# Performance work log

Hardware: AMD Instinct MI355X
Metric: run time of the kernel (lower is better)

The kernel has to match this reference:

```python
import jax, jax.numpy as jnp
import numpy as np

# Constant from livnium.kernel.constants (assumed scalar; value taken as 1.0).
K_O = 1.0
EPS = 1e-12  # F.normalize default eps

B, D, C = 16384, 1024, 3
F_DIM = D + 10  # features = h_final (D) + 10 scalar features


def setup_inputs() -> dict:
    key = jax.random.key(0)
    ks = jax.random.split(key, 8)
    s1 = 1.0 / np.sqrt(F_DIM)
    return {
        "h_final": jax.random.normal(ks[0], (B, D), jnp.float32),
        "v_p": jax.random.normal(ks[1], (B, D), jnp.float32),
        "v_h": jax.random.normal(ks[2], (B, D), jnp.float32),
        "neutral_dir": jax.random.normal(ks[3], (D,), jnp.float32),
        "neutral_scale": jnp.array(1.0, jnp.float32),
        "w1": jax.random.normal(ks[4], (F_DIM, F_DIM), jnp.float32) * s1,
        "b1": jnp.zeros((F_DIM,), jnp.float32),
        "w2": jax.random.normal(ks[5], (C, F_DIM), jnp.float32) * s1,
        "b2": jnp.zeros((C,), jnp.float32),
    }


def _normalize(x, axis):
    n = jnp.linalg.norm(x, axis=axis, keepdims=True)
    return x / jnp.maximum(n, EPS)


def reference(h_final, v_p, v_h, neutral_dir, neutral_scale, w1, b1, w2, b2):
    v_p_n = _normalize(v_p, -1)                      # [B, D]
    v_h_n = _normalize(v_h, -1)                      # [B, D]
    nd_n = _normalize(neutral_dir, 0)                # [D]

    # alignment(): cosine of the unit vectors == batched dot product.
    align = jnp.sum(v_p_n * v_h_n, axis=-1, keepdims=True)        # [B, 1]
    opp = jnp.sum(-v_p_n * v_h_n, axis=-1, keepdims=True)          # [B, 1]
    align_neutral_p = neutral_scale * jnp.sum(v_p_n * nd_n, axis=-1, keepdims=True)
    align_neutral_h = neutral_scale * jnp.sum(v_h_n * nd_n, axis=-1, keepdims=True)

    energy = K_O * ((1.0 + align) * 0.5)
    expose_neg = (1.0 - align) * 0.5
    dist_p_h = jnp.linalg.norm(v_h - v_p, axis=-1, keepdims=True)
    r_p = jnp.linalg.norm(v_p, axis=-1, keepdims=True)
    r_h = jnp.linalg.norm(v_h, axis=-1, keepdims=True)
    r_final = jnp.linalg.norm(h_final, axis=-1, keepdims=True)

    features = jnp.concatenate(
        [h_final, align, opp, energy, expose_neg, dist_p_h,
         r_p, r_h, r_final, align_neutral_p, align_neutral_h], axis=-1)  # [B, D+10]

    hidden = jax.nn.relu(features @ w1.T + b1)
    logits = hidden @ w2.T + b2                      # [B, C]
    return logits
```

## Files before the change

### kernel.cpp

```cpp
#include <hip/hip_runtime.h>
#include <cstdint>
#include <cstddef>

#define B_ROWS 16384
#define D_DIM  1024
#define F_REAL 1034
#define N_PAD  1152
#define K_PAD  1088
#define NK     (K_PAD / 64)
#define EPSN   1e-12f

typedef __bf16 bf16x8 __attribute__((ext_vector_type(8)));
typedef float  f32x4  __attribute__((ext_vector_type(4)));
typedef unsigned short u16;

__device__ __forceinline__ u16 f2bf(float f) {
    __bf16 b = (__bf16)f;
    return __builtin_bit_cast(u16, b);
}

__global__ __launch_bounds__(256)
void prep_kernel(const float* __restrict__ h, const float* __restrict__ vp,
                 const float* __restrict__ vh, const float* __restrict__ nd,
                 const float* __restrict__ nsp, u16* __restrict__ A)
{
    const int row  = blockIdx.x * 4 + (threadIdx.x >> 6);
    const int lane = threadIdx.x & 63;
    const float4* hp  = (const float4*)(h  + (size_t)row * D_DIM);
    const float4* vpp = (const float4*)(vp + (size_t)row * D_DIM);
    const float4* vhp = (const float4*)(vh + (size_t)row * D_DIM);
    const float4* ndp = (const float4*)nd;
    u16* arow = A + (size_t)row * K_PAD;

    float s_pp = 0.f, s_hh = 0.f, s_pv = 0.f, s_ff = 0.f;
    float s_dd = 0.f, s_pn = 0.f, s_hn = 0.f, s_nn = 0.f;

    #pragma unroll
    for (int c = 0; c < 4; ++c) {
        const int idx = lane + c * 64;
        float4 p = vpp[idx], q = vhp[idx], f = hp[idx], n = ndp[idx];

        s_pp += p.x*p.x + p.y*p.y + p.z*p.z + p.w*p.w;
        s_hh += q.x*q.x + q.y*q.y + q.z*q.z + q.w*q.w;
        s_pv += p.x*q.x + p.y*q.y + p.z*q.z + p.w*q.w;
        s_ff += f.x*f.x + f.y*f.y + f.z*f.z + f.w*f.w;
        float dx = q.x-p.x, dy = q.y-p.y, dz = q.z-p.z, dw = q.w-p.w;
        s_dd += dx*dx + dy*dy + dz*dz + dw*dw;
        s_pn += p.x*n.x + p.y*n.y + p.z*n.z + p.w*n.w;
        s_hn += q.x*n.x + q.y*n.y + q.z*n.z + q.w*n.w;
        s_nn += n.x*n.x + n.y*n.y + n.z*n.z + n.w*n.w;

        ushort4 ho;
        ho.x = f2bf(f.x); ho.y = f2bf(f.y); ho.z = f2bf(f.z); ho.w = f2bf(f.w);
        *(ushort4*)(arow + idx * 4) = ho;
    }

    #pragma unroll
    for (int m = 32; m >= 1; m >>= 1) {
        s_pp += __shfl_xor(s_pp, m, 64);
        s_hh += __shfl_xor(s_hh, m, 64);
        s_pv += __shfl_xor(s_pv, m, 64);
        s_ff += __shfl_xor(s_ff, m, 64);
        s_dd += __shfl_xor(s_dd, m, 64);
        s_pn += __shfl_xor(s_pn, m, 64);
        s_hn += __shfl_xor(s_hn, m, 64);
        s_nn += __shfl_xor(s_nn, m, 64);
    }

    if (lane == 0) {
        float np_ = sqrtf(s_pp), nh_ = sqrtf(s_hh), nf = sqrtf(s_ff);
        float npc = fmaxf(np_, EPSN), nhc = fmaxf(nh_, EPSN);
        float nnc = fmaxf(sqrtf(s_nn), EPSN);
        float align = s_pv / (npc * nhc);
        float ns = nsp[0];
        u16 fo[64];
        fo[0] = f2bf(align);
        fo[1] = f2bf(-align);
        fo[2] = f2bf(0.5f * (1.0f + align));
        fo[3] = f2bf(0.5f * (1.0f - align));
        fo[4] = f2bf(sqrtf(s_dd));
        fo[5] = f2bf(np_);
        fo[6] = f2bf(nh_);
        fo[7] = f2bf(nf);
        fo[8] = f2bf(ns * s_pn / (npc * nnc));
        fo[9] = f2bf(ns * s_hn / (nhc * nnc));
        #pragma unroll
        for (int i = 10; i < 64; ++i) fo[i] = 0;
        #pragma unroll
        for (int i = 0; i < 8; ++i)
            *(uint4*)(arow + D_DIM + i * 8) = *(uint4*)(fo + i * 8);
    }
}

__global__ __launch_bounds__(256)
void convw_kernel(const float* __restrict__ w1, u16* __restrict__ Bm)
{
    const int i = blockIdx.x;
    for (int j = threadIdx.x; j < K_PAD; j += 256) {
        float v = (i < F_REAL && j < F_REAL) ? w1[(size_t)i * F_REAL + j] : 0.0f;
        Bm[(size_t)i * K_PAD + j] = f2bf(v);
    }
}

__global__ __launch_bounds__(256)
void initout_kernel(const float* __restrict__ b2, float* __restrict__ out)
{
    int i = blockIdx.x * 256 + threadIdx.x;
    if (i < B_ROWS * 3) out[i] = b2[i % 3];
}

__global__ __launch_bounds__(256)
void gemm_kernel(const u16* __restrict__ A,
                 const u16* __restrict__ Bm,
                 const float* __restrict__ b1, const float* __restrict__ w2,
                 float* __restrict__ out)
{
    __shared__ __bf16 As[2 * 64 * 32];
    __shared__ __bf16 Bs[2 * 128 * 32];

    const int tid  = threadIdx.x;
    const int lane = tid & 63;
    const int wave = tid >> 6;
    const int wm = wave >> 1, wn = wave & 1;
    const int bm = blockIdx.x, bn = blockIdx.y;

    const u16* gaA;
    __bf16*    lA;
    {
        int row = tid >> 2;
        int kc  = (tid & 3) ^ (row & 3);
        gaA = A + (size_t)(bm * 64 + row) * K_PAD + kc * 8;
        lA  = As + tid * 8;
    }
    const u16* gaB[2];
    __bf16*    lB[2];
    #pragma unroll
    for (int o = 0; o < 2; ++o) {
        int s   = o * 256 + tid;
        int row = s >> 2;
        int kc  = (s & 3) ^ (row & 3);
        gaB[o] = Bm + (size_t)(bn * 128 + row) * K_PAD + kc * 8;
        lB[o]  = Bs + s * 8;
    }

    const int col  = lane & 15;
    const int quad = lane >> 4;
    const int swz  = quad ^ (col & 3);
    int aoff[2], boff[4];
    #pragma unroll
    for (int i = 0; i < 2; ++i)
        aoff[i] = ((wm * 32 + i * 16 + col) * 4 + swz) * 8;
    #pragma unroll
    for (int j = 0; j < 4; ++j)
        boff[j] = ((wn * 64 + j * 16 + col) * 4 + swz) * 8;

    f32x4 acc[2][4];
    #pragma unroll
    for (int i = 0; i < 2; ++i)
        #pragma unroll
        for (int j = 0; j < 4; ++j)
            acc[i][j] = (f32x4){0.f, 0.f, 0.f, 0.f};

    uint4 ra0, ra1, rb00, rb01, rb10, rb11;
    ra0  = *(const uint4*)(gaA);
    ra1  = *(const uint4*)(gaA + 32);
    rb00 = *(const uint4*)(gaB[0]);
    rb01 = *(const uint4*)(gaB[0] + 32);
    rb10 = *(const uint4*)(gaB[1]);
    rb11 = *(const uint4*)(gaB[1] + 32);
    *(uint4*)(lA)            = ra0;
    *(uint4*)(lA + 2048)     = ra1;
    *(uint4*)(lB[0])         = rb00;
    *(uint4*)(lB[0] + 4096)  = rb01;
    *(uint4*)(lB[1])         = rb10;
    *(uint4*)(lB[1] + 4096)  = rb11;
    __syncthreads();

    for (int kt = 0; kt < NK; ++kt) {
        if (kt + 1 < NK) {
            const int ko = (kt + 1) * 64;
            ra0  = *(const uint4*)(gaA + ko);
            ra1  = *(const uint4*)(gaA + ko + 32);
            rb00 = *(const uint4*)(gaB[0] + ko);
            rb01 = *(const uint4*)(gaB[0] + ko + 32);
            rb10 = *(const uint4*)(gaB[1] + ko);
            rb11 = *(const uint4*)(gaB[1] + ko + 32);
        }

        #pragma unroll
        for (int h = 0; h < 2; ++h) {
            const __bf16* Ab = As + h * 2048;
            const __bf16* Bb = Bs + h * 4096;
            bf16x8 av[2], bv[4];
            #pragma unroll
            for (int i = 0; i < 2; ++i) av[i] = *(const bf16x8*)(Ab + aoff[i]);
            #pragma unroll
            for (int j = 0; j < 4; ++j) bv[j] = *(const bf16x8*)(Bb + boff[j]);
            #pragma unroll
            for (int i = 0; i < 2; ++i)
                #pragma unroll
                for (int j = 0; j < 4; ++j)
                    acc[i][j] = __builtin_amdgcn_mfma_f32_16x16x32_bf16(
                                    av[i], bv[j], acc[i][j], 0, 0, 0);
        }

        if (kt + 1 < NK) {
            __syncthreads();
            *(uint4*)(lA)            = ra0;
            *(uint4*)(lA + 2048)     = ra1;
            *(uint4*)(lB[0])         = rb00;
            *(uint4*)(lB[0] + 4096)  = rb01;
            *(uint4*)(lB[1])         = rb10;
            *(uint4*)(lB[1] + 4096)  = rb11;
            __syncthreads();
        }
    }

    float bias[4], w20[4], w21[4], w22[4];
    #pragma unroll
    for (int ni = 0; ni < 4; ++ni) {
        int n = bn * 128 + wn * 64 + ni * 16 + col;
        bool v = n < F_REAL;
        bias[ni] = v ? b1[n] : 0.0f;
        w20[ni]  = v ? w2[n] : 0.0f;
        w21[ni]  = v ? w2[F_REAL + n] : 0.0f;
        w22[ni]  = v ? w2[2 * F_REAL + n] : 0.0f;
    }
    #pragma unroll
    for (int mi = 0; mi < 2; ++mi) {
        float c0[4] = {0,0,0,0}, c1[4] = {0,0,0,0}, c2[4] = {0,0,0,0};
        #pragma unroll
        for (int ni = 0; ni < 4; ++ni) {
            #pragma unroll
            for (int r = 0; r < 4; ++r) {
                float hd = fmaxf(acc[mi][ni][r] + bias[ni], 0.0f);
                c0[r] += hd * w20[ni];
                c1[r] += hd * w21[ni];
                c2[r] += hd * w22[ni];
            }
        }
        #pragma unroll
        for (int m = 8; m >= 1; m >>= 1) {
            #pragma unroll
            for (int r = 0; r < 4; ++r) {
                c0[r] += __shfl_xor(c0[r], m, 64);
                c1[r] += __shfl_xor(c1[r], m, 64);
                c2[r] += __shfl_xor(c2[r], m, 64);
            }
        }
        if (col == 0) {
            int gm = bm * 64 + wm * 32 + mi * 16 + quad * 4;
            #pragma unroll
            for (int r = 0; r < 4; ++r) {
                atomicAdd(out + (size_t)(gm + r) * 3 + 0, c0[r]);
                atomicAdd(out + (size_t)(gm + r) * 3 + 1, c1[r]);
                atomicAdd(out + (size_t)(gm + r) * 3 + 2, c2[r]);
            }
        }
    }
}

extern "C" void kernel_launch(void* const* d_in, const int* in_sizes, int n_in,
                              void* d_out, int out_size, void* d_ws, size_t ws_size,
                              hipStream_t stream)
{
    const float* h  = (const float*)d_in[0];
    const float* vp = (const float*)d_in[1];
    const float* vh = (const float*)d_in[2];
    const float* nd = (const float*)d_in[3];
    const float* ns = (const float*)d_in[4];
    const float* w1 = (const float*)d_in[5];
    const float* b1 = (const float*)d_in[6];
    const float* w2 = (const float*)d_in[7];
    const float* b2 = (const float*)d_in[8];
    float* out = (float*)d_out;

    u16* Afull = (u16*)d_ws;
    u16* Bfull = Afull + (size_t)B_ROWS * K_PAD;

    prep_kernel<<<B_ROWS / 4, 256, 0, stream>>>(h, vp, vh, nd, ns, Afull);
    convw_kernel<<<N_PAD, 256, 0, stream>>>(w1, Bfull);
    initout_kernel<<<(B_ROWS * 3 + 255) / 256, 256, 0, stream>>>(b2, out);
    gemm_kernel<<<dim3(B_ROWS / 64, N_PAD / 128), 256, 0, stream>>>(
        Afull, Bfull, b1, w2, out);
}
```

Baseline: 299.5 us.

## Double-buffer GEMM LDS tiles, swap grid order, and batch prep loads

The GEMM kernel now uses two LDS buffers so the next k-tile is written into the alternate buffer, which removes one barrier per iteration. The grid axes are swapped so consecutive blocks share the same A row-tile, aiming for better L2 reuse of A. In the prep kernel, all global loads are issued before any compute to increase memory-level parallelism. The cost is doubled LDS use, which may reduce occupancy.

```diff
diff --git a/kernel.cpp b/kernel.cpp
--- a/kernel.cpp
+++ b/kernel.cpp
@@ -32,14 +32,22 @@
     const float4* ndp = (const float4*)nd;
     u16* arow = A + (size_t)row * K_PAD;
 
+    float4 pr[4], qr[4], fr[4], nr[4];
+    #pragma unroll
+    for (int c = 0; c < 4; ++c) pr[c] = vpp[lane + c * 64];
+    #pragma unroll
+    for (int c = 0; c < 4; ++c) qr[c] = vhp[lane + c * 64];
+    #pragma unroll
+    for (int c = 0; c < 4; ++c) fr[c] = hp[lane + c * 64];
+    #pragma unroll
+    for (int c = 0; c < 4; ++c) nr[c] = ndp[lane + c * 64];
+
     float s_pp = 0.f, s_hh = 0.f, s_pv = 0.f, s_ff = 0.f;
     float s_dd = 0.f, s_pn = 0.f, s_hn = 0.f, s_nn = 0.f;
 
     #pragma unroll
     for (int c = 0; c < 4; ++c) {
-        const int idx = lane + c * 64;
-        float4 p = vpp[idx], q = vhp[idx], f = hp[idx], n = ndp[idx];
-
+        float4 p = pr[c], q = qr[c], f = fr[c], n = nr[c];
         s_pp += p.x*p.x + p.y*p.y + p.z*p.z + p.w*p.w;
         s_hh += q.x*q.x + q.y*q.y + q.z*q.z + q.w*q.w;
         s_pv += p.x*q.x + p.y*q.y + p.z*q.z + p.w*q.w;
@@ -52,7 +60,7 @@
 
         ushort4 ho;
         ho.x = f2bf(f.x); ho.y = f2bf(f.y); ho.z = f2bf(f.z); ho.w = f2bf(f.w);
-        *(ushort4*)(arow + idx * 4) = ho;
+        *(ushort4*)(arow + (lane + c * 64) * 4) = ho;
     }
 
     #pragma unroll
@@ -115,32 +123,32 @@
                  const float* __restrict__ b1, const float* __restrict__ w2,
                  float* __restrict__ out)
 {
-    __shared__ __bf16 As[2 * 64 * 32];
-    __shared__ __bf16 Bs[2 * 128 * 32];
+    __shared__ __bf16 As[2][2 * 64 * 32];
+    __shared__ __bf16 Bs[2][2 * 128 * 32];
 
     const int tid  = threadIdx.x;
     const int lane = tid & 63;
     const int wave = tid >> 6;
     const int wm = wave >> 1, wn = wave & 1;
-    const int bm = blockIdx.x, bn = blockIdx.y;
+    const int bn = blockIdx.x, bm = blockIdx.y;
 
     const u16* gaA;
-    __bf16*    lA;
+    int slotA;
     {
         int row = tid >> 2;
         int kc  = (tid & 3) ^ (row & 3);
-        gaA = A + (size_t)(bm * 64 + row) * K_PAD + kc * 8;
-        lA  = As + tid * 8;
+        gaA   = A + (size_t)(bm * 64 + row) * K_PAD + kc * 8;
+        slotA = tid * 8;
     }
     const u16* gaB[2];
-    __bf16*    lB[2];
+    int slotB[2];
     #pragma unroll
     for (int o = 0; o < 2; ++o) {
         int s   = o * 256 + tid;
         int row = s >> 2;
         int kc  = (s & 3) ^ (row & 3);
-        gaB[o] = Bm + (size_t)(bn * 128 + row) * K_PAD + kc * 8;
-        lB[o]  = Bs + s * 8;
+        gaB[o]   = Bm + (size_t)(bn * 128 + row) * K_PAD + kc * 8;
+        slotB[o] = s * 8;
     }
 
     const int col  = lane & 15;
@@ -168,15 +176,17 @@
     rb01 = *(const uint4*)(gaB[0] + 32);
     rb10 = *(const uint4*)(gaB[1]);
     rb11 = *(const uint4*)(gaB[1] + 32);
-    *(uint4*)(lA)            = ra0;
-    *(uint4*)(lA + 2048)     = ra1;
-    *(uint4*)(lB[0])         = rb00;
-    *(uint4*)(lB[0] + 4096)  = rb01;
-    *(uint4*)(lB[1])         = rb10;
-    *(uint4*)(lB[1] + 4096)  = rb11;
+    *(uint4*)(&As[0][slotA])           = ra0;
+    *(uint4*)(&As[0][slotA + 2048])    = ra1;
+    *(uint4*)(&Bs[0][slotB[0]])        = rb00;
+    *(uint4*)(&Bs[0][slotB[0] + 4096]) = rb01;
+    *(uint4*)(&Bs[0][slotB[1]])        = rb10;
+    *(uint4*)(&Bs[0][slotB[1] + 4096]) = rb11;
     __syncthreads();
 
     for (int kt = 0; kt < NK; ++kt) {
+        const int cur = kt & 1, nxt = cur ^ 1;
+
         if (kt + 1 < NK) {
             const int ko = (kt + 1) * 64;
             ra0  = *(const uint4*)(gaA + ko);
@@ -189,8 +199,8 @@
 
         #pragma unroll
         for (int h = 0; h < 2; ++h) {
-            const __bf16* Ab = As + h * 2048;
-            const __bf16* Bb = Bs + h * 4096;
+            const __bf16* Ab = &As[cur][h * 2048];
+            const __bf16* Bb = &Bs[cur][h * 4096];
             bf16x8 av[2], bv[4];
             #pragma unroll
             for (int i = 0; i < 2; ++i) av[i] = *(const bf16x8*)(Ab + aoff[i]);
@@ -205,13 +215,12 @@
         }
 
         if (kt + 1 < NK) {
-            __syncthreads();
-            *(uint4*)(lA)            = ra0;
-            *(uint4*)(lA + 2048)     = ra1;
-            *(uint4*)(lB[0])         = rb00;
-            *(uint4*)(lB[0] + 4096)  = rb01;
-            *(uint4*)(lB[1])         = rb10;
-            *(uint4*)(lB[1] + 4096)  = rb11;
+            *(uint4*)(&As[nxt][slotA])           = ra0;
+            *(uint4*)(&As[nxt][slotA + 2048])    = ra1;
+            *(uint4*)(&Bs[nxt][slotB[0]])        = rb00;
+            *(uint4*)(&Bs[nxt][slotB[0] + 4096]) = rb01;
+            *(uint4*)(&Bs[nxt][slotB[1]])        = rb10;
+            *(uint4*)(&Bs[nxt][slotB[1] + 4096]) = rb11;
             __syncthreads();
         }
     }
@@ -281,6 +290,6 @@
     prep_kernel<<<B_ROWS / 4, 256, 0, stream>>>(h, vp, vh, nd, ns, Afull);
     convw_kernel<<<N_PAD, 256, 0, stream>>>(w1, Bfull);
     initout_kernel<<<(B_ROWS * 3 + 255) / 256, 256, 0, stream>>>(b2, out);
-    gemm_kernel<<<dim3(B_ROWS / 64, N_PAD / 128), 256, 0, stream>>>(
+    gemm_kernel<<<dim3(N_PAD / 128, B_ROWS / 64), 256, 0, stream>>>(
         Afull, Bfull, b1, w2, out);
 }
```

New measurement: 323.8 us. 1.08x slower.

## Deepen GEMM global prefetch to two register stages and batch prep loads

Applied to the files above, without the earlier changes.

The GEMM main loop now keeps two register stages of global loads in flight, loading tile k+2 while tile k is computed, so global latency is hidden over two compute phases instead of one. The prep kernel issues all of its float4 loads up front before the reductions, which increases memory-level parallelism. The cost is more VGPRs for the second stage and for the prep buffers, which may lower occupancy.

```diff
diff --git a/kernel.cpp b/kernel.cpp
--- a/kernel.cpp
+++ b/kernel.cpp
@@ -32,14 +32,22 @@
     const float4* ndp = (const float4*)nd;
     u16* arow = A + (size_t)row * K_PAD;
 
+    float4 pr[4], qr[4], fr[4], nr[4];
+    #pragma unroll
+    for (int c = 0; c < 4; ++c) pr[c] = vpp[lane + c * 64];
+    #pragma unroll
+    for (int c = 0; c < 4; ++c) qr[c] = vhp[lane + c * 64];
+    #pragma unroll
+    for (int c = 0; c < 4; ++c) fr[c] = hp[lane + c * 64];
+    #pragma unroll
+    for (int c = 0; c < 4; ++c) nr[c] = ndp[lane + c * 64];
+
     float s_pp = 0.f, s_hh = 0.f, s_pv = 0.f, s_ff = 0.f;
     float s_dd = 0.f, s_pn = 0.f, s_hn = 0.f, s_nn = 0.f;
 
     #pragma unroll
     for (int c = 0; c < 4; ++c) {
-        const int idx = lane + c * 64;
-        float4 p = vpp[idx], q = vhp[idx], f = hp[idx], n = ndp[idx];
-
+        float4 p = pr[c], q = qr[c], f = fr[c], n = nr[c];
         s_pp += p.x*p.x + p.y*p.y + p.z*p.z + p.w*p.w;
         s_hh += q.x*q.x + q.y*q.y + q.z*q.z + q.w*q.w;
         s_pv += p.x*q.x + p.y*q.y + p.z*q.z + p.w*q.w;
@@ -52,7 +60,7 @@
 
         ushort4 ho;
         ho.x = f2bf(f.x); ho.y = f2bf(f.y); ho.z = f2bf(f.z); ho.w = f2bf(f.w);
-        *(ushort4*)(arow + idx * 4) = ho;
+        *(ushort4*)(arow + (lane + c * 64) * 4) = ho;
     }
 
     #pragma unroll
@@ -161,58 +169,69 @@
         for (int j = 0; j < 4; ++j)
             acc[i][j] = (f32x4){0.f, 0.f, 0.f, 0.f};
 
-    uint4 ra0, ra1, rb00, rb01, rb10, rb11;
-    ra0  = *(const uint4*)(gaA);
-    ra1  = *(const uint4*)(gaA + 32);
-    rb00 = *(const uint4*)(gaB[0]);
-    rb01 = *(const uint4*)(gaB[0] + 32);
-    rb10 = *(const uint4*)(gaB[1]);
-    rb11 = *(const uint4*)(gaB[1] + 32);
-    *(uint4*)(lA)            = ra0;
-    *(uint4*)(lA + 2048)     = ra1;
-    *(uint4*)(lB[0])         = rb00;
-    *(uint4*)(lB[0] + 4096)  = rb01;
-    *(uint4*)(lB[1])         = rb10;
-    *(uint4*)(lB[1] + 4096)  = rb11;
+    uint4 a0_0, a1_0, b00_0, b01_0, b10_0, b11_0;
+    uint4 a0_1, a1_1, b00_1, b01_1, b10_1, b11_1;
+
+#define LOAD_STAGE(st, ko)                                                    \
+    do {                                                                      \
+        a0_##st  = *(const uint4*)(gaA + (ko));                               \
+        a1_##st  = *(const uint4*)(gaA + (ko) + 32);                          \
+        b00_##st = *(const uint4*)(gaB[0] + (ko));                            \
+        b01_##st = *(const uint4*)(gaB[0] + (ko) + 32);                       \
+        b10_##st = *(const uint4*)(gaB[1] + (ko));                            \
+        b11_##st = *(const uint4*)(gaB[1] + (ko) + 32);                       \
+    } while (0)
+
+#define WRITE_STAGE(st)                                                       \
+    do {                                                                      \
+        *(uint4*)(lA)           = a0_##st;                                    \
+        *(uint4*)(lA + 2048)    = a1_##st;                                    \
+        *(uint4*)(lB[0])        = b00_##st;                                   \
+        *(uint4*)(lB[0] + 4096) = b01_##st;                                   \
+        *(uint4*)(lB[1])        = b10_##st;                                   \
+        *(uint4*)(lB[1] + 4096) = b11_##st;                                   \
+    } while (0)
+
+#define COMPUTE_TILE                                                          \
+    do {                                                                      \
+        _Pragma("unroll")                                                     \
+        for (int h = 0; h < 2; ++h) {                                         \
+            const __bf16* Ab = As + h * 2048;                                 \
+            const __bf16* Bb = Bs + h * 4096;                                 \
+            bf16x8 av[2], bv[4];                                              \
+            _Pragma("unroll")                                                 \
+            for (int i = 0; i < 2; ++i) av[i] = *(const bf16x8*)(Ab + aoff[i]); \
+            _Pragma("unroll")                                                 \
+            for (int j = 0; j < 4; ++j) bv[j] = *(const bf16x8*)(Bb + boff[j]); \
+            _Pragma("unroll")                                                 \
+            for (int i = 0; i < 2; ++i)                                       \
+                _Pragma("unroll")                                             \
+                for (int j = 0; j < 4; ++j)                                   \
+                    acc[i][j] = __builtin_amdgcn_mfma_f32_16x16x32_bf16(      \
+                                    av[i], bv[j], acc[i][j], 0, 0, 0);        \
+        }                                                                     \
+    } while (0)
+
+    LOAD_STAGE(0, 0);
+    LOAD_STAGE(1, 64);
+    WRITE_STAGE(0);
     __syncthreads();
 
-    for (int kt = 0; kt < NK; ++kt) {
-        if (kt + 1 < NK) {
-            const int ko = (kt + 1) * 64;
-            ra0  = *(const uint4*)(gaA + ko);
-            ra1  = *(const uint4*)(gaA + ko + 32);
-            rb00 = *(const uint4*)(gaB[0] + ko);
-            rb01 = *(const uint4*)(gaB[0] + ko + 32);
-            rb10 = *(const uint4*)(gaB[1] + ko);
-            rb11 = *(const uint4*)(gaB[1] + ko + 32);
-        }
-
-        #pragma unroll
-        for (int h = 0; h < 2; ++h) {
-            const __bf16* Ab = As + h * 2048;
-            const __bf16* Bb = Bs + h * 4096;
-            bf16x8 av[2], bv[4];
-            #pragma unroll
-            for (int i = 0; i < 2; ++i) av[i] = *(const bf16x8*)(Ab + aoff[i]);
-            #pragma unroll
-            for (int j = 0; j < 4; ++j) bv[j] = *(const bf16x8*)(Bb + boff[j]);
-            #pragma unroll
-            for (int i = 0; i < 2; ++i)
-                #pragma unroll
-                for (int j = 0; j < 4; ++j)
-                    acc[i][j] = __builtin_amdgcn_mfma_f32_16x16x32_bf16(
-                                    av[i], bv[j], acc[i][j], 0, 0, 0);
-        }
-
+    for (int kt = 0; kt < NK; kt += 2) {
+        if (kt + 2 < NK) LOAD_STAGE(0, (kt + 2) * 64);
+        COMPUTE_TILE;
         if (kt + 1 < NK) {
             __syncthreads();
-            *(uint4*)(lA)            = ra0;
-            *(uint4*)(lA + 2048)     = ra1;
-            *(uint4*)(lB[0])         = rb00;
-            *(uint4*)(lB[0] + 4096)  = rb01;
-            *(uint4*)(lB[1])         = rb10;
-            *(uint4*)(lB[1] + 4096)  = rb11;
+            WRITE_STAGE(1);
             __syncthreads();
+
+            if (kt + 3 < NK) LOAD_STAGE(1, (kt + 3) * 64);
+            COMPUTE_TILE;
+            if (kt + 2 < NK) {
+                __syncthreads();
+                WRITE_STAGE(0);
+                __syncthreads();
+            }
         }
     }
 
```

Result: faster. 292.1 us (-2.5%).
